# Kernel optimization log

Hardware: AMD Instinct MI355X
Metric: run time of the kernel (lower is better)

## Reference

```python
import jax, jax.numpy as jnp
import numpy as np

N_GENES = 20000
N_PATHWAYS = 512
D_EMBED = 128
N_HEADS = 4
N_LAYERS = 2
B, G = 16, 2000


def setup_inputs() -> dict:
    key = jax.random.key(0)
    ks = jax.random.split(key, 20)
    s = 0.02
    inp = {
        "gene_indices": jax.random.randint(ks[0], (B, G), 0, N_GENES),
        "expression_values": jax.random.uniform(ks[1], (B, G), dtype=jnp.float32),
        "pathway_indices": jax.random.randint(ks[2], (B, N_PATHWAYS), 0, N_PATHWAYS),
        "W_soft": jax.random.normal(ks[3], (N_GENES, N_PATHWAYS), jnp.float32) * 0.1,
        "gene_emb": jax.random.normal(ks[4], (N_GENES, D_EMBED), jnp.float32) * s,
        "pathway_emb": jax.random.normal(ks[5], (N_PATHWAYS, D_EMBED), jnp.float32) * s,
        "Wq": jax.random.normal(ks[6], (N_LAYERS, D_EMBED, D_EMBED), jnp.float32) * s,
        "bq": jnp.zeros((N_LAYERS, D_EMBED), jnp.float32),
        "Wk": jax.random.normal(ks[7], (N_LAYERS, D_EMBED, D_EMBED), jnp.float32) * s,
        "bk": jnp.zeros((N_LAYERS, D_EMBED), jnp.float32),
        "Wv": jax.random.normal(ks[8], (N_LAYERS, D_EMBED, D_EMBED), jnp.float32) * s,
        "bv": jnp.zeros((N_LAYERS, D_EMBED), jnp.float32),
        "Wo": jax.random.normal(ks[9], (N_LAYERS, D_EMBED, D_EMBED), jnp.float32) * s,
        "bo": jnp.zeros((N_LAYERS, D_EMBED), jnp.float32),
        "W_out": jax.random.normal(ks[10], (D_EMBED, N_PATHWAYS), jnp.float32) * s,
        "b_out": jnp.zeros((N_PATHWAYS,), jnp.float32),
    }
    return inp


def reference(gene_indices, expression_values, pathway_indices, W_soft,
              gene_emb, pathway_emb, Wq, bq, Wk, bk, Wv, bv, Wo, bo,
              W_out, b_out):
    Bb, Gg = gene_indices.shape
    L, D, _ = Wq.shape
    H = N_HEADS
    dh = D // H
    # soft gene-pathway mask: note original indexes gene_indices[1] (row 1) for all batches
    M = jax.nn.sigmoid(W_soft[gene_indices[1]])[None, None]  # (1,1,G,P)
    # gene embeddings modulated by expression values
    x = gene_emb[gene_indices] * expression_values[..., None]  # (B,G,D)
    kx = pathway_emb[pathway_indices]                          # (B,P,D)
    Pp = kx.shape[1]
    inv_sqrt = 1.0 / jnp.sqrt(jnp.asarray(dh, x.dtype))
    for l in range(L):
        Q = (x @ Wq[l] + bq[l]).reshape(Bb, Gg, H, dh).transpose(0, 2, 1, 3)
        K = (kx @ Wk[l] + bk[l]).reshape(Bb, Pp, H, dh).transpose(0, 2, 1, 3)
        V = (kx @ Wv[l] + bv[l]).reshape(Bb, Pp, H, dh).transpose(0, 2, 1, 3)
        scores = jnp.einsum('bhqd,bhkd->bhqk', Q, K) * inv_sqrt
        scores = scores * M  # soft multiplicative sigmoid gating before softmax
        attn = jax.nn.softmax(scores, axis=-1)
        o = jnp.einsum('bhqk,bhkd->bhqd', attn, V).transpose(0, 2, 1, 3).reshape(Bb, Gg, D)
        x = o @ Wo[l] + bo[l]
    pathway_scores = x.mean(axis=1) @ W_out + b_out  # (B, n_pathways)
    return pathway_scores
```

## Files before the change

kernel.cpp:

```cpp
#include <hip/hip_runtime.h>
#include <hip/hip_bf16.h>


typedef __attribute__((ext_vector_type(8))) short s16x8;
typedef __attribute__((ext_vector_type(4))) float f32x4;

static __device__ __forceinline__ unsigned short f2bf(float f) {
  union { float f; unsigned u; } v; v.f = f;
  unsigned r = v.u + 0x7fff + ((v.u >> 16) & 1);
  return (unsigned short)(r >> 16);
}
static __device__ __forceinline__ unsigned cvtpk(float lo, float hi) {
  unsigned r;
  asm("v_cvt_pk_bf16_f32 %0, %1, %2" : "=v"(r) : "v"(lo), "v"(hi));
  return r;
}
static __device__ __forceinline__ float exp2a(float x) {
  float r;
  asm("v_exp_f32 %0, %1" : "=v"(r) : "v"(x));
  return r;
}
static __device__ __forceinline__ float ub2f(unsigned w, int r) {
  return (float)((w >> (8 * r)) & 0xffu);
}
static __device__ __forceinline__ s16x8 pack4(unsigned a, unsigned b, unsigned c, unsigned d) {
  union { unsigned u[4]; s16x8 v; } t;
  t.u[0] = a; t.u[1] = b; t.u[2] = c; t.u[3] = d;
  return t.v;
}
static __device__ __forceinline__ void gll16(const void* g, void* l) {
  __builtin_amdgcn_global_load_lds((const __attribute__((address_space(1))) void*)g,
                                   (__attribute__((address_space(3))) void*)l, 16, 0, 0);
}

__global__ void prep_wt(const float* __restrict__ Wq, const float* __restrict__ Wk,
                        const float* __restrict__ Wv, const float* __restrict__ Wo,
                        unsigned short* __restrict__ WtAll) {
  int id = blockIdx.x;
  int l = id >> 2, type = id & 3;
  const float* W = (type == 0 ? Wq : type == 1 ? Wk : type == 2 ? Wv : Wo) + l * 16384;
  unsigned short* dst = WtAll + id * 16384;
  for (int i = threadIdx.x; i < 16384; i += 256) {
    int k, n;
    if (type == 1 || type == 2) { n = i >> 7; k = i & 127; }
    else {
      int t = i >> 9, lane = (i >> 3) & 63, j = i & 7;
      int nt = t >> 2, c = t & 3, lg = lane >> 4, gg = lane & 15;
      k = c * 32 + lg * 4 + (j & 3) + 16 * (j >> 2);
      n = nt * 16 + gg;
    }
    dst[i] = f2bf(W[k * 128 + n]);
  }
}

__global__ void prep_gate(const int* __restrict__ gene_idx, const float* __restrict__ W_soft,
                          unsigned char* __restrict__ Mgu) {
  int t = blockIdx.x * 256 + threadIdx.x;
  int g = t >> 5, sub = (t >> 2) & 7, lg = t & 3;
  int idx = gene_idx[2000 + g];
  const float* src = &W_soft[(size_t)idx * 512 + sub * 64 + lg * 8];
  float4 v0 = *(const float4*)&src[0];
  float4 v1 = *(const float4*)&src[4];
  float4 v2 = *(const float4*)&src[32];
  float4 v3 = *(const float4*)&src[36];
  unsigned char tmp[16];
  const float* vs[4] = {&v0.x, &v1.x, &v2.x, &v3.x};
#pragma unroll
  for (int tl = 0; tl < 4; tl++)
#pragma unroll
    for (int r = 0; r < 4; r++)
      tmp[tl * 4 + r] = (unsigned char)rintf(255.f / (1.f + __expf(-vs[tl][r])));
  *(uint4*)(Mgu + (size_t)g * 512 + sub * 64 + lg * 16) = *(const uint4*)tmp;
}

__global__ __launch_bounds__(64) void kv_pack(const int* __restrict__ pw_idx,
                                              const float* __restrict__ pw_emb,
                                              const unsigned short* __restrict__ WtAll,
                                              const float* __restrict__ bk,
                                              const float* __restrict__ bv,
                                              unsigned short* __restrict__ KfG,
                                              unsigned short* __restrict__ VfG) {
  int bx = blockIdx.x;
  int l = bx >> 10, rest = bx & 1023;
  int b = rest >> 6, r2 = rest & 63;
  int pt = r2 >> 1, dh2 = r2 & 1;
  const unsigned short* WtK = WtAll + (l * 4 + 1) * 16384;
  const unsigned short* WtV = WtAll + (l * 4 + 2) * 16384;
  const float* bkl = bk + l * 128;
  const float* bvl = bv + l * 128;
  int lane = threadIdx.x, lg = lane >> 4, gg = lane & 15;
  int p = pt * 16 + gg;
  int pi = pw_idx[b * 512 + p];
  const float* src = pw_emb + (size_t)pi * 128 + lg * 8;
  s16x8 kxf[4];
#pragma unroll
  for (int c = 0; c < 4; ++c) {
    float4 u0 = *(const float4*)&src[c * 32];
    float4 u1 = *(const float4*)&src[c * 32 + 4];
    kxf[c] = pack4(cvtpk(u0.x, u0.y), cvtpk(u0.z, u0.w), cvtpk(u1.x, u1.y), cvtpk(u1.z, u1.w));
  }
  int tg = 4 * (p >> 6) + 2 * ((p >> 5) & 1) + ((p >> 2) & 1);
  int q  = 4 * ((p >> 3) & 3) + (p & 3);
#pragma unroll
  for (int dtl = 0; dtl < 4; ++dtl) {
    int dt = dh2 * 4 + dtl;
    f32x4 acc = (f32x4){0.f, 0.f, 0.f, 0.f};
#pragma unroll
    for (int c = 0; c < 4; ++c) {
      s16x8 wf = *(const s16x8*)&WtK[(size_t)(16 * dt + gg) * 128 + c * 32 + lg * 8];
      acc = __builtin_amdgcn_mfma_f32_16x16x32_bf16(wf, kxf[c], acc, 0, 0, 0);
    }
    float4 b4 = *(const float4*)&bkl[16 * dt + 4 * lg];
    int h = dt >> 1, u = dt & 1;
    size_t addr = ((((size_t)l * 16 + b) * 4 + h) * 32 + tg) * 512 + (lg * 16 + q) * 8 + 4 * u;
    uint2 st;
    st.x = cvtpk(acc[0] + b4.x, acc[1] + b4.y);
    st.y = cvtpk(acc[2] + b4.z, acc[3] + b4.w);
    *(uint2*)&KfG[addr] = st;
  }
  int cV = pt >> 1, lgpp = 2 * (pt & 1) + (lg >> 1);
#pragma unroll
  for (int ntl = 0; ntl < 4; ++ntl) {
    int nt = dh2 * 4 + ntl;
    f32x4 acc = (f32x4){0.f, 0.f, 0.f, 0.f};
#pragma unroll
    for (int c = 0; c < 4; ++c) {
      s16x8 wf = *(const s16x8*)&WtV[(size_t)(16 * nt + gg) * 128 + c * 32 + lg * 8];
      acc = __builtin_amdgcn_mfma_f32_16x16x32_bf16(kxf[c], wf, acc, 0, 0, 0);
    }
    float bvv = bvl[16 * nt + gg];
    int h = nt >> 1, half = nt & 1;
    size_t addr = (((((size_t)l * 16 + b) * 4 + h) * 2 + half) * 16 + cV) * 512 + (lgpp * 16 + gg) * 8 + 4 * (lg & 1);
    uint2 st;
    st.x = cvtpk(acc[0] + bvv, acc[1] + bvv);
    st.y = cvtpk(acc[2] + bvv, acc[3] + bvv);
    *(uint2*)&VfG[addr] = st;
  }
}

static __device__ __forceinline__ void stage_chunk(
    const unsigned short* __restrict__ KfG, const unsigned short* __restrict__ VfG,
    unsigned short* lds0, int buf, int l, int b, int h, int kc, int wave, int lane) {
  unsigned short* base = lds0 + buf * 16384 + wave * 8 * 512;
  if (wave < 2) {
    const unsigned short* src =
        KfG + ((((size_t)l * 16 + b) * 4 + h) * 32 + kc * 16 + wave * 8) * 512 + lane * 8;
#pragma unroll
    for (int i = 0; i < 8; ++i) gll16(src + i * 512, base + i * 512);
  } else {
    int half = wave - 2;
    const unsigned short* src =
        VfG + (((((size_t)l * 16 + b) * 4 + h) * 2 + half) * 16 + kc * 8) * 512 + lane * 8;
#pragma unroll
    for (int i = 0; i < 8; ++i) gll16(src + i * 512, base + i * 512);
  }
}

#define SCSTEP(MM, SC)                                                          \
  {                                                                             \
    unsigned gw0 = gu[((MM) & 1) * 4 + (SC)].x;                                 \
    unsigned gw1 = gu[((MM) & 1) * 4 + (SC)].y;                                 \
    unsigned gw2 = gu[((MM) & 1) * 4 + (SC)].z;                                 \
    unsigned gw3 = gu[((MM) & 1) * 4 + (SC)].w;                                 \
    f32x4 av0 = __builtin_amdgcn_mfma_f32_16x16x32_bf16(                        \
        *(const s16x8*)&KL[((SC) * 4 + 0) * 512 + lane * 8], qf[(MM) >> 1], zf, 0, 0, 0); \
    f32x4 av1 = __builtin_amdgcn_mfma_f32_16x16x32_bf16(                        \
        *(const s16x8*)&KL[((SC) * 4 + 1) * 512 + lane * 8], qf[(MM) >> 1], zf, 0, 0, 0); \
    f32x4 av2 = __builtin_amdgcn_mfma_f32_16x16x32_bf16(                        \
        *(const s16x8*)&KL[((SC) * 4 + 2) * 512 + lane * 8], qf[(MM) >> 1], zf, 0, 0, 0); \
    f32x4 av3 = __builtin_amdgcn_mfma_f32_16x16x32_bf16(                        \
        *(const s16x8*)&KL[((SC) * 4 + 3) * 512 + lane * 8], qf[(MM) >> 1], zf, 0, 0, 0); \
    float e0, e1, e2, e3;                                                       \
    unsigned p00, p01, p10, p11, p20, p21, p30, p31;                            \
    e0 = exp2a(av0[0] * ub2f(gw0, 0));                                          \
    e1 = exp2a(av0[1] * ub2f(gw0, 1));                                          \
    e2 = exp2a(av0[2] * ub2f(gw0, 2));                                          \
    e3 = exp2a(av0[3] * ub2f(gw0, 3));                                          \
    sums[(MM) >> 1] += (e0 + e1) + (e2 + e3);                                   \
    p00 = cvtpk(e0, e1); p01 = cvtpk(e2, e3);                                   \
    e0 = exp2a(av1[0] * ub2f(gw1, 0));                                          \
    e1 = exp2a(av1[1] * ub2f(gw1, 1));                                          \
    e2 = exp2a(av1[2] * ub2f(gw1, 2));                                          \
    e3 = exp2a(av1[3] * ub2f(gw1, 3));                                          \
    sums[(MM) >> 1] += (e0 + e1) + (e2 + e3);                                   \
    p10 = cvtpk(e0, e1); p11 = cvtpk(e2, e3);                                   \
    e0 = exp2a(av2[0] * ub2f(gw2, 0));                                          \
    e1 = exp2a(av2[1] * ub2f(gw2, 1));                                          \
    e2 = exp2a(av2[2] * ub2f(gw2, 2));                                          \
    e3 = exp2a(av2[3] * ub2f(gw2, 3));                                          \
    sums[(MM) >> 1] += (e0 + e1) + (e2 + e3);                                   \
    p20 = cvtpk(e0, e1); p21 = cvtpk(e2, e3);                                   \
    e0 = exp2a(av3[0] * ub2f(gw3, 0));                                          \
    e1 = exp2a(av3[1] * ub2f(gw3, 1));                                          \
    e2 = exp2a(av3[2] * ub2f(gw3, 2));                                          \
    e3 = exp2a(av3[3] * ub2f(gw3, 3));                                          \
    sums[(MM) >> 1] += (e0 + e1) + (e2 + e3);                                   \
    p30 = cvtpk(e0, e1); p31 = cvtpk(e2, e3);                                   \
    s16x8 pf0 = pack4(p00, p01, p10, p11);                                      \
    s16x8 pf1 = pack4(p20, p21, p30, p31);                                      \
    ov[(MM) >> 1][0] = __builtin_amdgcn_mfma_f32_16x16x32_bf16(                 \
        *(const s16x8*)&VL[((SC) * 2 + 0) * 512 + lane * 8], pf0, ov[(MM) >> 1][0], 0, 0, 0); \
    ov[(MM) >> 1][1] = __builtin_amdgcn_mfma_f32_16x16x32_bf16(                 \
        *(const s16x8*)&VL[(8 + (SC) * 2 + 0) * 512 + lane * 8], pf0, ov[(MM) >> 1][1], 0, 0, 0); \
    ov[(MM) >> 1][0] = __builtin_amdgcn_mfma_f32_16x16x32_bf16(                 \
        *(const s16x8*)&VL[((SC) * 2 + 1) * 512 + lane * 8], pf1, ov[(MM) >> 1][0], 0, 0, 0); \
    ov[(MM) >> 1][1] = __builtin_amdgcn_mfma_f32_16x16x32_bf16(                 \
        *(const s16x8*)&VL[(8 + (SC) * 2 + 1) * 512 + lane * 8], pf1, ov[(MM) >> 1][1], 0, 0, 0); \
  }

#define CHUNK(MM)                                                               \
  {                                                                             \
    if ((MM) < 7) {                                                             \
      stage_chunk(KfG, VfG, lds0, ((MM) + 1) & 1, l, b, ((MM) + 1) >> 1,        \
                  ((MM) + 1) & 1, wave, lane);                                  \
      asm volatile("s_waitcnt vmcnt(8)" ::: "memory");                          \
    } else {                                                                    \
      asm volatile("s_waitcnt vmcnt(0)" ::: "memory");                          \
    }                                                                           \
    __builtin_amdgcn_s_barrier();                                               \
    __builtin_amdgcn_sched_barrier(0);                                          \
    const unsigned short* KL = &lds[(MM) & 1][0];                               \
    const unsigned short* VL = &lds[(MM) & 1][8192];                            \
    SCSTEP(MM, 0) SCSTEP(MM, 1) SCSTEP(MM, 2) SCSTEP(MM, 3)                     \
    __builtin_amdgcn_sched_barrier(0);                                          \
    __builtin_amdgcn_s_barrier();                                               \
  }

#define FINH(H)                                                                 \
  {                                                                             \
    float s = sums[H];                                                          \
    s += __shfl_xor(s, 16, 64);                                                 \
    s += __shfl_xor(s, 32, 64);                                                 \
    float inv = 1.f / s;                                                        \
    pfO[H] = pack4(cvtpk(ov[H][0][0] * inv, ov[H][0][1] * inv),                 \
                   cvtpk(ov[H][0][2] * inv, ov[H][0][3] * inv),                 \
                   cvtpk(ov[H][1][0] * inv, ov[H][1][1] * inv),                 \
                   cvtpk(ov[H][1][2] * inv, ov[H][1][3] * inv));                \
  }

__global__ __launch_bounds__(256, 2) void mega_kern(
    const int* __restrict__ gene_idx, const float* __restrict__ expr,
    const float* __restrict__ gene_emb, const unsigned short* __restrict__ WtAll,
    const float* __restrict__ bq, const float* __restrict__ bo,
    const unsigned short* __restrict__ KfG, const unsigned short* __restrict__ VfG,
    const unsigned char* __restrict__ Mgu, float* __restrict__ partial) {
  __shared__ unsigned short lds[2][16384];
  int bid = blockIdx.x;
  int xcd = bid & 7, wi = bid >> 3;
  int b = xcd * 2 + (wi >> 5);
  int gt = wi & 31;
  int tid = threadIdx.x, lane = tid & 63, wave = tid >> 6;
  int lg = lane >> 4, gg = lane & 15;
  int grow = gt * 64 + wave * 16 + gg;
  int growc = grow < 2000 ? grow : 1999;
  int row = b * 2000 + growc;
  const f32x4 zf = (f32x4){0.f, 0.f, 0.f, 0.f};
  const float GQ = 0.17677669529663687f * 1.4426950408889634f / 255.f;

  uint4 gu[8];
  {
    const unsigned char* gbase = Mgu + (size_t)growc * 512 + lg * 16;
#pragma unroll
    for (int sub = 0; sub < 8; ++sub)
      gu[sub] = *(const uint4*)(gbase + sub * 64);
  }
  s16x8 xf[4];
  {
    int gi = gene_idx[row];
    float ev = expr[row];
    const float* src = gene_emb + (size_t)gi * 128 + lg * 4;
#pragma unroll
    for (int c = 0; c < 4; ++c) {
      float4 u0 = *(const float4*)&src[c * 32];
      float4 u1 = *(const float4*)&src[c * 32 + 16];
      xf[c] = pack4(cvtpk(u0.x * ev, u0.y * ev), cvtpk(u0.z * ev, u0.w * ev),
                    cvtpk(u1.x * ev, u1.y * ev), cvtpk(u1.z * ev, u1.w * ev));
    }
  }

  unsigned short* lds0 = &lds[0][0];

#pragma unroll 1
  for (int l = 0; l < 2; ++l) {
    const unsigned short* WqFl = WtAll + (l * 4 + 0) * 16384;
    const unsigned short* WoFl = WtAll + (l * 4 + 3) * 16384;
    const float* bql = bq + l * 128;
    const float* bol = bo + l * 128;

    stage_chunk(KfG, VfG, lds0, 0, l, b, 0, 0, wave, lane);

    s16x8 qf[4];
    {
      f32x4 qacc[8];
#pragma unroll
      for (int nt = 0; nt < 8; ++nt) {
        f32x4 acc = zf;
#pragma unroll
        for (int c = 0; c < 4; ++c) {
          s16x8 wf = *(const s16x8*)&WqFl[((nt * 4 + c) << 9) + lane * 8];
          acc = __builtin_amdgcn_mfma_f32_16x16x32_bf16(wf, xf[c], acc, 0, 0, 0);
        }
        float4 b4 = *(const float4*)&bql[nt * 16 + lg * 4];
        acc[0] = (acc[0] + b4.x) * GQ;
        acc[1] = (acc[1] + b4.y) * GQ;
        acc[2] = (acc[2] + b4.z) * GQ;
        acc[3] = (acc[3] + b4.w) * GQ;
        qacc[nt] = acc;
      }
#pragma unroll
      for (int h = 0; h < 4; ++h)
        qf[h] = pack4(cvtpk(qacc[2 * h][0], qacc[2 * h][1]), cvtpk(qacc[2 * h][2], qacc[2 * h][3]),
                      cvtpk(qacc[2 * h + 1][0], qacc[2 * h + 1][1]), cvtpk(qacc[2 * h + 1][2], qacc[2 * h + 1][3]));
    }

    f32x4 ov[4][2];
    float sums[4];
#pragma unroll
    for (int h = 0; h < 4; ++h) {
      ov[h][0] = zf;
      ov[h][1] = zf;
      sums[h] = 0.f;
    }
    s16x8 pfO[4];

    CHUNK(0) CHUNK(1) FINH(0)
    CHUNK(2) CHUNK(3) FINH(1)
    CHUNK(4) CHUNK(5) FINH(2)
    CHUNK(6) CHUNK(7) FINH(3)

    f32x4 xacc[8];
#pragma unroll
    for (int nt = 0; nt < 8; ++nt) {
      f32x4 acc = zf;
#pragma unroll
      for (int c = 0; c < 4; ++c) {
        s16x8 wf = *(const s16x8*)&WoFl[((nt * 4 + c) << 9) + lane * 8];
        acc = __builtin_amdgcn_mfma_f32_16x16x32_bf16(wf, pfO[c], acc, 0, 0, 0);
      }
      float4 b4 = *(const float4*)&bol[nt * 16 + lg * 4];
      acc[0] += b4.x; acc[1] += b4.y; acc[2] += b4.z; acc[3] += b4.w;
      xacc[nt] = acc;
    }

    if (l == 0) {
#pragma unroll
      for (int c = 0; c < 4; ++c)
        xf[c] = pack4(cvtpk(xacc[2 * c][0], xacc[2 * c][1]), cvtpk(xacc[2 * c][2], xacc[2 * c][3]),
                      cvtpk(xacc[2 * c + 1][0], xacc[2 * c + 1][1]), cvtpk(xacc[2 * c + 1][2], xacc[2 * c + 1][3]));
    } else {
      if (grow >= 2000) {
#pragma unroll
        for (int nt = 0; nt < 8; ++nt) xacc[nt] = zf;
      }
#pragma unroll
      for (int nt = 0; nt < 8; ++nt) {
#pragma unroll
        for (int msk = 1; msk <= 8; msk <<= 1) {
          xacc[nt][0] += __shfl_xor(xacc[nt][0], msk, 64);
          xacc[nt][1] += __shfl_xor(xacc[nt][1], msk, 64);
          xacc[nt][2] += __shfl_xor(xacc[nt][2], msk, 64);
          xacc[nt][3] += __shfl_xor(xacc[nt][3], msk, 64);
        }
      }
      float* red = (float*)lds0;
      if (gg == 0) {
#pragma unroll
        for (int nt = 0; nt < 8; ++nt) {
          red[wave * 128 + nt * 16 + lg * 4 + 0] = xacc[nt][0];
          red[wave * 128 + nt * 16 + lg * 4 + 1] = xacc[nt][1];
          red[wave * 128 + nt * 16 + lg * 4 + 2] = xacc[nt][2];
          red[wave * 128 + nt * 16 + lg * 4 + 3] = xacc[nt][3];
        }
      }
      __syncthreads();
      if (tid < 128) {
        float s = red[tid] + red[128 + tid] + red[256 + tid] + red[384 + tid];
        partial[((size_t)b * 32 + gt) * 128 + tid] = s;
      }
    }
  }
}

__global__ void final_out(const float* __restrict__ partial, const float* __restrict__ W_out,
                          const float* __restrict__ b_out, float* __restrict__ out) {
  int b = blockIdx.x, tid = threadIdx.x;
  __shared__ float mean[128];
  if (tid < 128) {
    float s = 0.f;
    for (int c = 0; c < 32; c++) s += partial[((size_t)b * 32 + c) * 128 + tid];
    mean[tid] = s * (1.f / 2000.f);
  }
  __syncthreads();
  for (int p = tid; p < 512; p += 256) {
    float a = b_out[p];
    for (int d = 0; d < 128; d++) a += mean[d] * W_out[d * 512 + p];
    out[b * 512 + p] = a;
  }
}

extern "C" void kernel_launch(void* const* d_in, const int* in_sizes, int n_in,
                              void* d_out, int out_size, void* d_ws, size_t ws_size,
                              hipStream_t stream) {
  const int*   gene_idx = (const int*)d_in[0];
  const float* expr     = (const float*)d_in[1];
  const int*   pw_idx   = (const int*)d_in[2];
  const float* W_soft   = (const float*)d_in[3];
  const float* gene_emb = (const float*)d_in[4];
  const float* pw_emb   = (const float*)d_in[5];
  const float* Wq = (const float*)d_in[6];
  const float* bq = (const float*)d_in[7];
  const float* Wk = (const float*)d_in[8];
  const float* bk = (const float*)d_in[9];
  const float* Wv = (const float*)d_in[10];
  const float* bv = (const float*)d_in[11];
  const float* Wo = (const float*)d_in[12];
  const float* bo = (const float*)d_in[13];
  const float* W_out = (const float*)d_in[14];
  const float* b_out = (const float*)d_in[15];
  float* out = (float*)d_out;

  char* ws = (char*)d_ws;
  size_t off = 0;
  auto alloc = [&](size_t bytes) {
    char* p = ws + off;
    off += (bytes + 255) & ~(size_t)255;
    return p;
  };
  unsigned char*  Mgu   = (unsigned char*)alloc((size_t)2048 * 512);
  unsigned short* WtAll = (unsigned short*)alloc((size_t)8 * 16384 * 2);
  unsigned short* KfG   = (unsigned short*)alloc((size_t)2 * 16 * 4 * 32 * 512 * 2);
  unsigned short* VfG   = (unsigned short*)alloc((size_t)2 * 16 * 4 * 2 * 16 * 512 * 2);
  float* partial        = (float*)alloc((size_t)16 * 32 * 128 * 4);

  prep_wt<<<8, 256, 0, stream>>>(Wq, Wk, Wv, Wo, WtAll);
  prep_gate<<<250, 256, 0, stream>>>(gene_idx, W_soft, Mgu);
  kv_pack<<<2048, 64, 0, stream>>>(pw_idx, pw_emb, WtAll, bk, bv, KfG, VfG);
  mega_kern<<<512, 256, 0, stream>>>(gene_idx, expr, gene_emb, WtAll, bq, bo, KfG, VfG, Mgu, partial);
  final_out<<<16, 256, 0, stream>>>(partial, W_out, b_out, out);
}
```

Before: 109.9 us.

## Replace LDS-staged K/V pipeline with single-wave blocks reading K/V fragments from global

The attention mega-kernel moves from 256-thread blocks that double-buffer K/V chunks into LDS with barriers to 64-thread single-wave blocks (2000 blocks) that load K/V MFMA fragments directly from global/L2. Padding rows and the in-block LDS reduction go away, and each wave writes its partial sums straight to a larger partial buffer that final_out reduces over 125 slices. This removes LDS staging, barrier overhead and tail padding. In exchange, K/V data is no longer shared across four waves through LDS, so global/L2 traffic rises and load latency becomes exposed.

```diff
diff --git a/kernel.cpp b/kernel.cpp
--- a/kernel.cpp
+++ b/kernel.cpp
@@ -27,10 +27,6 @@
   union { unsigned u[4]; s16x8 v; } t;
   t.u[0] = a; t.u[1] = b; t.u[2] = c; t.u[3] = d;
   return t.v;
-}
-static __device__ __forceinline__ void gll16(const void* g, void* l) {
-  __builtin_amdgcn_global_load_lds((const __attribute__((address_space(1))) void*)g,
-                                   (__attribute__((address_space(3))) void*)l, 16, 0, 0);
 }
 
 __global__ void prep_wt(const float* __restrict__ Wq, const float* __restrict__ Wk,
@@ -138,23 +134,10 @@
   }
 }
 
-static __device__ __forceinline__ void stage_chunk(
-    const unsigned short* __restrict__ KfG, const unsigned short* __restrict__ VfG,
-    unsigned short* lds0, int buf, int l, int b, int h, int kc, int wave, int lane) {
-  unsigned short* base = lds0 + buf * 16384 + wave * 8 * 512;
-  if (wave < 2) {
-    const unsigned short* src =
-        KfG + ((((size_t)l * 16 + b) * 4 + h) * 32 + kc * 16 + wave * 8) * 512 + lane * 8;
-#pragma unroll
-    for (int i = 0; i < 8; ++i) gll16(src + i * 512, base + i * 512);
-  } else {
-    int half = wave - 2;
-    const unsigned short* src =
-        VfG + (((((size_t)l * 16 + b) * 4 + h) * 2 + half) * 16 + kc * 8) * 512 + lane * 8;
-#pragma unroll
-    for (int i = 0; i < 8; ++i) gll16(src + i * 512, base + i * 512);
-  }
-}
+#define KAT(MM, SC, TL) \
+  (*(const s16x8*)(kfb + ((((MM) >> 1) * 32 + ((MM) & 1) * 16 + (SC) * 4 + (TL)) * 512)))
+#define VAT(MM, SC, CC, HALF) \
+  (*(const s16x8*)(vfb + (((((MM) >> 1) * 2 + (HALF)) * 16 + ((MM) & 1) * 8 + (SC) * 2 + (CC)) * 512)))
 
 #define SCSTEP(MM, SC)                                                          \
   {                                                                             \
@@ -162,14 +145,10 @@
     unsigned gw1 = gu[((MM) & 1) * 4 + (SC)].y;                                 \
     unsigned gw2 = gu[((MM) & 1) * 4 + (SC)].z;                                 \
     unsigned gw3 = gu[((MM) & 1) * 4 + (SC)].w;                                 \
-    f32x4 av0 = __builtin_amdgcn_mfma_f32_16x16x32_bf16(                        \
-        *(const s16x8*)&KL[((SC) * 4 + 0) * 512 + lane * 8], qf[(MM) >> 1], zf, 0, 0, 0); \
-    f32x4 av1 = __builtin_amdgcn_mfma_f32_16x16x32_bf16(                        \
-        *(const s16x8*)&KL[((SC) * 4 + 1) * 512 + lane * 8], qf[(MM) >> 1], zf, 0, 0, 0); \
-    f32x4 av2 = __builtin_amdgcn_mfma_f32_16x16x32_bf16(                        \
-        *(const s16x8*)&KL[((SC) * 4 + 2) * 512 + lane * 8], qf[(MM) >> 1], zf, 0, 0, 0); \
-    f32x4 av3 = __builtin_amdgcn_mfma_f32_16x16x32_bf16(                        \
-        *(const s16x8*)&KL[((SC) * 4 + 3) * 512 + lane * 8], qf[(MM) >> 1], zf, 0, 0, 0); \
+    f32x4 av0 = __builtin_amdgcn_mfma_f32_16x16x32_bf16(KAT(MM, SC, 0), qf[(MM) >> 1], zf, 0, 0, 0); \
+    f32x4 av1 = __builtin_amdgcn_mfma_f32_16x16x32_bf16(KAT(MM, SC, 1), qf[(MM) >> 1], zf, 0, 0, 0); \
+    f32x4 av2 = __builtin_amdgcn_mfma_f32_16x16x32_bf16(KAT(MM, SC, 2), qf[(MM) >> 1], zf, 0, 0, 0); \
+    f32x4 av3 = __builtin_amdgcn_mfma_f32_16x16x32_bf16(KAT(MM, SC, 3), qf[(MM) >> 1], zf, 0, 0, 0); \
     float e0, e1, e2, e3;                                                       \
     unsigned p00, p01, p10, p11, p20, p21, p30, p31;                            \
     e0 = exp2a(av0[0] * ub2f(gw0, 0));                                          \
@@ -198,33 +177,13 @@
     p30 = cvtpk(e0, e1); p31 = cvtpk(e2, e3);                                   \
     s16x8 pf0 = pack4(p00, p01, p10, p11);                                      \
     s16x8 pf1 = pack4(p20, p21, p30, p31);                                      \
-    ov[(MM) >> 1][0] = __builtin_amdgcn_mfma_f32_16x16x32_bf16(                 \
-        *(const s16x8*)&VL[((SC) * 2 + 0) * 512 + lane * 8], pf0, ov[(MM) >> 1][0], 0, 0, 0); \
-    ov[(MM) >> 1][1] = __builtin_amdgcn_mfma_f32_16x16x32_bf16(                 \
-        *(const s16x8*)&VL[(8 + (SC) * 2 + 0) * 512 + lane * 8], pf0, ov[(MM) >> 1][1], 0, 0, 0); \
-    ov[(MM) >> 1][0] = __builtin_amdgcn_mfma_f32_16x16x32_bf16(                 \
-        *(const s16x8*)&VL[((SC) * 2 + 1) * 512 + lane * 8], pf1, ov[(MM) >> 1][0], 0, 0, 0); \
-    ov[(MM) >> 1][1] = __builtin_amdgcn_mfma_f32_16x16x32_bf16(                 \
-        *(const s16x8*)&VL[(8 + (SC) * 2 + 1) * 512 + lane * 8], pf1, ov[(MM) >> 1][1], 0, 0, 0); \
-  }
-
-#define CHUNK(MM)                                                               \
-  {                                                                             \
-    if ((MM) < 7) {                                                             \
-      stage_chunk(KfG, VfG, lds0, ((MM) + 1) & 1, l, b, ((MM) + 1) >> 1,        \
-                  ((MM) + 1) & 1, wave, lane);                                  \
-      asm volatile("s_waitcnt vmcnt(8)" ::: "memory");                          \
-    } else {                                                                    \
-      asm volatile("s_waitcnt vmcnt(0)" ::: "memory");                          \
-    }                                                                           \
-    __builtin_amdgcn_s_barrier();                                               \
-    __builtin_amdgcn_sched_barrier(0);                                          \
-    const unsigned short* KL = &lds[(MM) & 1][0];                               \
-    const unsigned short* VL = &lds[(MM) & 1][8192];                            \
-    SCSTEP(MM, 0) SCSTEP(MM, 1) SCSTEP(MM, 2) SCSTEP(MM, 3)                     \
-    __builtin_amdgcn_sched_barrier(0);                                          \
-    __builtin_amdgcn_s_barrier();                                               \
-  }
+    ov[(MM) >> 1][0] = __builtin_amdgcn_mfma_f32_16x16x32_bf16(VAT(MM, SC, 0, 0), pf0, ov[(MM) >> 1][0], 0, 0, 0); \
+    ov[(MM) >> 1][1] = __builtin_amdgcn_mfma_f32_16x16x32_bf16(VAT(MM, SC, 0, 1), pf0, ov[(MM) >> 1][1], 0, 0, 0); \
+    ov[(MM) >> 1][0] = __builtin_amdgcn_mfma_f32_16x16x32_bf16(VAT(MM, SC, 1, 0), pf1, ov[(MM) >> 1][0], 0, 0, 0); \
+    ov[(MM) >> 1][1] = __builtin_amdgcn_mfma_f32_16x16x32_bf16(VAT(MM, SC, 1, 1), pf1, ov[(MM) >> 1][1], 0, 0, 0); \
+  }
+
+#define CHUNK(MM) { SCSTEP(MM, 0) SCSTEP(MM, 1) SCSTEP(MM, 2) SCSTEP(MM, 3) }
 
 #define FINH(H)                                                                 \
   {                                                                             \
@@ -238,28 +197,25 @@
                    cvtpk(ov[H][1][2] * inv, ov[H][1][3] * inv));                \
   }
 
-__global__ __launch_bounds__(256, 2) void mega_kern(
+__global__ __launch_bounds__(64, 2) void mega_kern(
     const int* __restrict__ gene_idx, const float* __restrict__ expr,
     const float* __restrict__ gene_emb, const unsigned short* __restrict__ WtAll,
     const float* __restrict__ bq, const float* __restrict__ bo,
     const unsigned short* __restrict__ KfG, const unsigned short* __restrict__ VfG,
     const unsigned char* __restrict__ Mgu, float* __restrict__ partial) {
-  __shared__ unsigned short lds[2][16384];
   int bid = blockIdx.x;
-  int xcd = bid & 7, wi = bid >> 3;
-  int b = xcd * 2 + (wi >> 5);
-  int gt = wi & 31;
-  int tid = threadIdx.x, lane = tid & 63, wave = tid >> 6;
+  int b = (bid & 7) * 2 + ((bid >> 3) & 1);
+  int gt = bid >> 4;
+  int lane = threadIdx.x & 63;
   int lg = lane >> 4, gg = lane & 15;
-  int grow = gt * 64 + wave * 16 + gg;
-  int growc = grow < 2000 ? grow : 1999;
-  int row = b * 2000 + growc;
+  int grow = gt * 16 + gg;
+  int row = b * 2000 + grow;
   const f32x4 zf = (f32x4){0.f, 0.f, 0.f, 0.f};
   const float GQ = 0.17677669529663687f * 1.4426950408889634f / 255.f;
 
   uint4 gu[8];
   {
-    const unsigned char* gbase = Mgu + (size_t)growc * 512 + lg * 16;
+    const unsigned char* gbase = Mgu + (size_t)grow * 512 + lg * 16;
 #pragma unroll
     for (int sub = 0; sub < 8; ++sub)
       gu[sub] = *(const uint4*)(gbase + sub * 64);
@@ -278,16 +234,14 @@
     }
   }
 
-  unsigned short* lds0 = &lds[0][0];
-
 #pragma unroll 1
   for (int l = 0; l < 2; ++l) {
-    const unsigned short* WqFl = WtAll + (l * 4 + 0) * 16384;
-    const unsigned short* WoFl = WtAll + (l * 4 + 3) * 16384;
+    const unsigned short* WqFl = WtAll + (l * 4 + 0) * 16384 + lane * 8;
+    const unsigned short* WoFl = WtAll + (l * 4 + 3) * 16384 + lane * 8;
     const float* bql = bq + l * 128;
     const float* bol = bo + l * 128;
-
-    stage_chunk(KfG, VfG, lds0, 0, l, b, 0, 0, wave, lane);
+    const unsigned short* kfb = KfG + ((size_t)(l * 16 + b) * 4) * 32 * 512 + lane * 8;
+    const unsigned short* vfb = VfG + ((size_t)(l * 16 + b) * 8) * 16 * 512 + lane * 8;
 
     s16x8 qf[4];
     {
@@ -297,7 +251,7 @@
         f32x4 acc = zf;
 #pragma unroll
         for (int c = 0; c < 4; ++c) {
-          s16x8 wf = *(const s16x8*)&WqFl[((nt * 4 + c) << 9) + lane * 8];
+          s16x8 wf = *(const s16x8*)&WqFl[(nt * 4 + c) << 9];
           acc = __builtin_amdgcn_mfma_f32_16x16x32_bf16(wf, xf[c], acc, 0, 0, 0);
         }
         float4 b4 = *(const float4*)&bql[nt * 16 + lg * 4];
@@ -334,7 +288,7 @@
       f32x4 acc = zf;
 #pragma unroll
       for (int c = 0; c < 4; ++c) {
-        s16x8 wf = *(const s16x8*)&WoFl[((nt * 4 + c) << 9) + lane * 8];
+        s16x8 wf = *(const s16x8*)&WoFl[(nt * 4 + c) << 9];
         acc = __builtin_amdgcn_mfma_f32_16x16x32_bf16(wf, pfO[c], acc, 0, 0, 0);
       }
       float4 b4 = *(const float4*)&bol[nt * 16 + lg * 4];
@@ -348,10 +302,6 @@
         xf[c] = pack4(cvtpk(xacc[2 * c][0], xacc[2 * c][1]), cvtpk(xacc[2 * c][2], xacc[2 * c][3]),
                       cvtpk(xacc[2 * c + 1][0], xacc[2 * c + 1][1]), cvtpk(xacc[2 * c + 1][2], xacc[2 * c + 1][3]));
     } else {
-      if (grow >= 2000) {
-#pragma unroll
-        for (int nt = 0; nt < 8; ++nt) xacc[nt] = zf;
-      }
 #pragma unroll
       for (int nt = 0; nt < 8; ++nt) {
 #pragma unroll
@@ -362,20 +312,14 @@
           xacc[nt][3] += __shfl_xor(xacc[nt][3], msk, 64);
         }
       }
-      float* red = (float*)lds0;
       if (gg == 0) {
+        float* dst = partial + ((size_t)b * 125 + gt) * 128;
 #pragma unroll
         for (int nt = 0; nt < 8; ++nt) {
-          red[wave * 128 + nt * 16 + lg * 4 + 0] = xacc[nt][0];
-          red[wave * 128 + nt * 16 + lg * 4 + 1] = xacc[nt][1];
-          red[wave * 128 + nt * 16 + lg * 4 + 2] = xacc[nt][2];
-          red[wave * 128 + nt * 16 + lg * 4 + 3] = xacc[nt][3];
+          float4 st;
+          st.x = xacc[nt][0]; st.y = xacc[nt][1]; st.z = xacc[nt][2]; st.w = xacc[nt][3];
+          *(float4*)&dst[nt * 16 + lg * 4] = st;
         }
-      }
-      __syncthreads();
-      if (tid < 128) {
-        float s = red[tid] + red[128 + tid] + red[256 + tid] + red[384 + tid];
-        partial[((size_t)b * 32 + gt) * 128 + tid] = s;
       }
     }
   }
@@ -387,7 +331,7 @@
   __shared__ float mean[128];
   if (tid < 128) {
     float s = 0.f;
-    for (int c = 0; c < 32; c++) s += partial[((size_t)b * 32 + c) * 128 + tid];
+    for (int c = 0; c < 125; c++) s += partial[((size_t)b * 125 + c) * 128 + tid];
     mean[tid] = s * (1.f / 2000.f);
   }
   __syncthreads();
@@ -430,11 +374,11 @@
   unsigned short* WtAll = (unsigned short*)alloc((size_t)8 * 16384 * 2);
   unsigned short* KfG   = (unsigned short*)alloc((size_t)2 * 16 * 4 * 32 * 512 * 2);
   unsigned short* VfG   = (unsigned short*)alloc((size_t)2 * 16 * 4 * 2 * 16 * 512 * 2);
-  float* partial        = (float*)alloc((size_t)16 * 32 * 128 * 4);
+  float* partial        = (float*)alloc((size_t)16 * 125 * 128 * 4);
 
   prep_wt<<<8, 256, 0, stream>>>(Wq, Wk, Wv, Wo, WtAll);
   prep_gate<<<250, 256, 0, stream>>>(gene_idx, W_soft, Mgu);
   kv_pack<<<2048, 64, 0, stream>>>(pw_idx, pw_emb, WtAll, bk, bv, KfG, VfG);
-  mega_kern<<<512, 256, 0, stream>>>(gene_idx, expr, gene_emb, WtAll, bq, bo, KfG, VfG, Mgu, partial);
+  mega_kern<<<2000, 64, 0, stream>>>(gene_idx, expr, gene_emb, WtAll, bq, bo, KfG, VfG, Mgu, partial);
   final_out<<<16, 256, 0, stream>>>(partial, W_out, b_out, out);
 }
```

After: 171.6 us. 1.56x slower.
